# Optimization experiments

Measured on AMD Instinct MI355X. Metric: run time of the kernel, lower is better.

Reference implementation:

```python
import jax, jax.numpy as jnp
import numpy as np

B, S, H, F, E, K, NS = 2, 2048, 2048, 768, 32, 4, 8
SZ = F // NS  # secondary expert size (96)
CAP = 2 * (B * S) * K // E


def setup_inputs() -> dict:
    key = jax.random.key(0)
    k = jax.random.split(key, 7)
    s = 0.02
    return {
        "router_input": jax.random.normal(k[0], (B, S, H), jnp.float32),
        "hidden_states": jax.random.normal(k[1], (B, S, H), jnp.float32),
        "w_router": jax.random.normal(k[2], (H, E), jnp.float32) * s,
        "w_up": jax.random.normal(k[3], (E, H, F), jnp.float32) * s,
        "w_gate": jax.random.normal(k[4], (E, H, F), jnp.float32) * s,
        "w_down": jax.random.normal(k[5], (E, F, H), jnp.float32) * s,
        "w_sgate": jax.random.normal(k[6], (E, H, NS), jnp.float32) * s,
    }


def reference(router_input, hidden_states, w_router, w_up, w_gate, w_down, w_sgate):
    b, s, h = hidden_states.shape
    x = hidden_states.reshape(-1, h)          # [T,H]
    r = router_input.reshape(-1, h)           # [T,H] (early router input)
    T = x.shape[0]

    # top-k routing (early router, softmax over top-k logits)
    logits = r @ w_router                     # [T,E]
    top_logits, sel = jax.lax.top_k(logits, K)  # [T,K]
    rw = jax.nn.softmax(top_logits.astype(jnp.float32), axis=-1).astype(x.dtype)

    # combined per-(expert, token) routing weight and hit mask
    onehot = jax.nn.one_hot(sel, E, dtype=x.dtype)      # [T,K,E]
    wmat = (onehot * rw[..., None]).sum(1).T            # [E,T]
    mask = onehot.sum(1).T                              # [E,T] in {0,1}

    # fixed-capacity dispatch: per expert gather up to CAP routed tokens
    valid, idx = jax.lax.top_k(mask, CAP)               # [E,CAP]
    w = jnp.take_along_axis(wmat, idx, axis=1) * valid  # [E,CAP]

    xe = x[idx]                                         # [E,CAP,H]
    re = r[idx]                                         # [E,CAP,H]

    # hierarchical MLP: secondary gate (hard sigmoid>0.5) over NS groups
    sg = (jax.nn.sigmoid(jnp.einsum('ech,ehs->ecs', re, w_sgate)) > 0.5).astype(x.dtype)
    act = jnp.einsum('ech,ehf->ecf', xe, w_up) * jax.nn.relu(jnp.einsum('ech,ehf->ecf', xe, w_gate))
    act = (act.reshape(E, CAP, NS, SZ) * sg[..., None]).reshape(E, CAP, F)
    out = jnp.einsum('ecf,efh->ech', act, w_down) * w[..., None]  # weighted combine

    # scatter-accumulate back to tokens (invalid slots have zero weight)
    final = jnp.zeros((T, h), x.dtype).at[idx.reshape(-1)].add(out.reshape(-1, h))
    return final.reshape(b, s, h), top_logits
```

## Files before the change

kernel.cpp:

```cpp
#include <hip/hip_runtime.h>

#define TT 4096
#define HD 2048
#define FD 768
#define NE 32
#define TOPK 4
#define NSG 8
#define CAPE 1024
#define MAXTILES 160
#define UPGRID (MAXTILES * 12)
#define DNGRID (MAXTILES * 16)

typedef __attribute__((ext_vector_type(8))) short short8;
typedef __attribute__((ext_vector_type(4))) float f32x4;
typedef __attribute__((ext_vector_type(4))) unsigned short us4;
typedef __attribute__((ext_vector_type(8))) unsigned short us8;

__device__ __forceinline__ unsigned short f2bf(float f) {
  unsigned u = __builtin_bit_cast(unsigned, f);
  u += 0x7FFFu + ((u >> 16) & 1u);
  return (unsigned short)(u >> 16);
}
__device__ __forceinline__ float bf2f(unsigned short b) {
  return __builtin_bit_cast(float, (unsigned)b << 16);
}

__device__ __forceinline__ void async16(const void* g, void* l) {
  __builtin_amdgcn_global_load_lds(
      (const __attribute__((address_space(1))) unsigned int*)g,
      (__attribute__((address_space(3))) unsigned int*)l, 16, 0, 0);
}

__global__ __launch_bounds__(256) void wrt_kernel(const float* __restrict__ w_router,
                                                  float* __restrict__ wrt) {
  int idx = blockIdx.x * 256 + threadIdx.x;
  int e = idx >> 11, h = idx & 2047;
  wrt[idx] = w_router[h * NE + e];
}

#define LSTR 68
__global__ __launch_bounds__(256) void logits_kernel(
    const float* __restrict__ rin, const float* __restrict__ wrt,
    float* __restrict__ logits) {
  __shared__ float As[16 * LSTR];
  __shared__ float Bs[32 * LSTR];
  const int tid = threadIdx.x;
  const int t0 = blockIdx.x * 16;
  const int tp = tid >> 4, eg = tid & 15;
  f32x4 acc0 = (f32x4)0.f, acc1 = (f32x4)0.f;
  for (int kt = 0; kt < HD; kt += 64) {
    __syncthreads();
    {
      int row = tid >> 4, col = (tid & 15) * 4;
      *(f32x4*)&As[row * LSTR + col] =
          *(const f32x4*)&rin[(size_t)(t0 + row) * HD + kt + col];
    }
    {
      int e = tid >> 3, col = (tid & 7) * 8;
      *(f32x4*)&Bs[e * LSTR + col] = *(const f32x4*)&wrt[(size_t)e * HD + kt + col];
      *(f32x4*)&Bs[e * LSTR + col + 4] =
          *(const f32x4*)&wrt[(size_t)e * HD + kt + col + 4];
    }
    __syncthreads();
#pragma unroll
    for (int k4 = 0; k4 < 16; ++k4) {
      f32x4 a = *(const f32x4*)&As[tp * LSTR + k4 * 4];
      f32x4 b0 = *(const f32x4*)&Bs[eg * LSTR + k4 * 4];
      f32x4 b1 = *(const f32x4*)&Bs[(eg + 16) * LSTR + k4 * 4];
      acc0 += a * b0;
      acc1 += a * b1;
    }
  }
  logits[(t0 + tp) * NE + eg] = acc0[0] + acc0[1] + acc0[2] + acc0[3];
  logits[(t0 + tp) * NE + eg + 16] = acc1[0] + acc1[1] + acc1[2] + acc1[3];
}

__global__ __launch_bounds__(256) void topk_kernel(
    const float* __restrict__ logits, float* __restrict__ top_logits,
    int* __restrict__ sel, float* __restrict__ rwts) {
  __shared__ float lg[256 * 33];
  const int tid = threadIdx.x;
  const int t0 = blockIdx.x * 256;
#pragma unroll
  for (int i = 0; i < 8; ++i) {
    int fi = tid + i * 256;
    f32x4 v = *(const f32x4*)&logits[(size_t)t0 * NE + fi * 4];
    int tok = fi >> 3, e0 = (fi & 7) * 4;
#pragma unroll
    for (int c = 0; c < 4; ++c) lg[tok * 33 + e0 + c] = v[c];
  }
  __syncthreads();
  const float* row = &lg[tid * 33];
  float val[TOPK];
  int idx[TOPK];
  unsigned used = 0;
#pragma unroll
  for (int k = 0; k < TOPK; ++k) {
    float best = -1e30f;
    int bi = 0;
    for (int e = 0; e < NE; ++e) {
      float v = row[e];
      if (!((used >> e) & 1u) && v > best) { best = v; bi = e; }
    }
    used |= 1u << bi;
    val[k] = best;
    idx[k] = bi;
  }
  float ex[TOPK], sum = 0.f;
#pragma unroll
  for (int k = 0; k < TOPK; ++k) { ex[k] = expf(val[k] - val[0]); sum += ex[k]; }
  int t = t0 + tid;
#pragma unroll
  for (int k = 0; k < TOPK; ++k) {
    top_logits[t * TOPK + k] = val[k];
    sel[t * TOPK + k] = idx[k];
    rwts[t * TOPK + k] = ex[k] / sum;
  }
}

__global__ __launch_bounds__(256) void dispatch_kernel(
    const int* __restrict__ sel, const float* __restrict__ rwts,
    int* __restrict__ tok_idx, float* __restrict__ tok_w, int* __restrict__ counts,
    int* __restrict__ slotmap) {
  const int e = blockIdx.x;
  __shared__ int wcnt[4];
  __shared__ int base;
  const int tid = threadIdx.x, lane = tid & 63, wid = tid >> 6;
  if (tid == 0) base = 0;
  __syncthreads();
  for (int t0 = 0; t0 < TT; t0 += 256) {
    int t = t0 + tid;
    int hitk = -1;
#pragma unroll
    for (int k = 0; k < TOPK; ++k)
      if (sel[t * TOPK + k] == e) hitk = k;
    unsigned long long m = __ballot(hitk >= 0);
    if (lane == 0) wcnt[wid] = __popcll(m);
    __syncthreads();
    int off = base;
    for (int w = 0; w < wid; ++w) off += wcnt[w];
    int pos = off + __popcll(m & ((1ULL << lane) - 1ULL));
    if (hitk >= 0) {
      if (pos < CAPE) {
        tok_idx[e * CAPE + pos] = t;
        tok_w[e * CAPE + pos] = rwts[t * TOPK + hitk];
        slotmap[t * TOPK + hitk] = e * CAPE + pos;
      } else {
        slotmap[t * TOPK + hitk] = -1;
      }
    }
    __syncthreads();
    if (tid == 0) base += wcnt[0] + wcnt[1] + wcnt[2] + wcnt[3];
    __syncthreads();
  }
  if (tid == 0) counts[e] = base < CAPE ? base : CAPE;
}

__global__ void build_tiles_kernel(const int* __restrict__ counts,
                                   int* __restrict__ tlist, int* __restrict__ ntiles) {
  if (threadIdx.x == 0) {
    int n = 0;
    for (int e = 0; e < NE; ++e) {
      int c = counts[e];
      int mb = (c + 127) >> 7;
      for (int m = 0; m < mb; ++m) tlist[n++] = (e << 8) | m;
    }
    ntiles[0] = n;
  }
}

__global__ __launch_bounds__(256) void sgate_kernel(
    const float* __restrict__ rin, const float* __restrict__ w_sgate,
    const int* __restrict__ tok_idx, const int* __restrict__ counts,
    unsigned* __restrict__ sgbits) {
  const int e = blockIdx.y;
  const int count = counts[e];
  const int s0 = blockIdx.x * 128;
  if (s0 >= count || count == 0) return;
  __shared__ float wsgS[2048 * 9];
  const int tid = threadIdx.x, lane = tid & 63, wid = tid >> 6;
  const float* wsg = w_sgate + (size_t)e * (HD * NSG);
#pragma unroll
  for (int p = 0; p < 8; ++p) {
    int row = p * 256 + tid;
    f32x4 v0 = *(const f32x4*)&wsg[row * 8];
    f32x4 v1 = *(const f32x4*)&wsg[row * 8 + 4];
#pragma unroll
    for (int c = 0; c < 4; ++c) {
      wsgS[row * 9 + c] = v0[c];
      wsgS[row * 9 + 4 + c] = v1[c];
    }
  }
  __syncthreads();
  const int base = s0 + wid * 32;
  for (int j = 0; j < 16; ++j) {
    int sA = base + j, sB = base + j + 16;
    if (sA >= count) break;
    int tokA = tok_idx[e * CAPE + sA];
    int tokB = tok_idx[e * CAPE + (sB < count ? sB : sA)];
    float zA[8], zB[8];
#pragma unroll
    for (int s = 0; s < 8; ++s) { zA[s] = 0.f; zB[s] = 0.f; }
    const float* rAp = rin + (size_t)tokA * HD;
    const float* rBp = rin + (size_t)tokB * HD;
#pragma unroll 4
    for (int i = 0; i < 32; ++i) {
      int h = lane + 64 * i;
      float rA = rAp[h];
      float rB = rBp[h];
#pragma unroll
      for (int s = 0; s < 8; ++s) {
        float w = wsgS[h * 9 + s];
        zA[s] += rA * w;
        zB[s] += rB * w;
      }
    }
#pragma unroll
    for (int s = 0; s < 8; ++s) {
#pragma unroll
      for (int d = 1; d < 64; d <<= 1) {
        zA[s] += __shfl_xor(zA[s], d);
        zB[s] += __shfl_xor(zB[s], d);
      }
    }
    if (lane == 0) {
      unsigned bA = 0, bB = 0;
#pragma unroll
      for (int s = 0; s < 8; ++s) {
        bA |= ((unsigned)(zA[s] > 0.f)) << s;
        bB |= ((unsigned)(zB[s] > 0.f)) << s;
      }
      sgbits[e * CAPE + sA] = bA;
      if (sB < count) sgbits[e * CAPE + sB] = bB;
    }
  }
}

__global__ __launch_bounds__(256) void cvt_x_kernel(const float* __restrict__ x,
                                                    unsigned short* __restrict__ xb) {
  size_t i = ((size_t)blockIdx.x * 256 + threadIdx.x) * 8;
  float4 a = *(const float4*)(x + i);
  float4 b = *(const float4*)(x + i + 4);
  us8 o = {f2bf(a.x), f2bf(a.y), f2bf(a.z), f2bf(a.w),
           f2bf(b.x), f2bf(b.y), f2bf(b.z), f2bf(b.w)};
  *(us8*)(xb + i) = o;
}

__global__ __launch_bounds__(256) void transpose_cvt_kernel(
    const float* __restrict__ in, unsigned short* __restrict__ out, int R, int C) {
  const int e = blockIdx.z;
  const int r0 = blockIdx.x * 64, c0 = blockIdx.y * 64;
  __shared__ float t[64][65];
  const int tid = threadIdx.x;
  const float* inp = in + (size_t)e * R * C;
  {
    const int row = tid >> 4, col4 = (tid & 15) << 2;
#pragma unroll
    for (int p = 0; p < 4; ++p) {
      float4 v = *(const float4*)(inp + (size_t)(r0 + p * 16 + row) * C + c0 + col4);
      t[p * 16 + row][col4 + 0] = v.x;
      t[p * 16 + row][col4 + 1] = v.y;
      t[p * 16 + row][col4 + 2] = v.z;
      t[p * 16 + row][col4 + 3] = v.w;
    }
  }
  __syncthreads();
  {
    const int c = tid >> 2, j = tid & 3;
    us8 o0, o1;
#pragma unroll
    for (int i = 0; i < 8; ++i) o0[i] = f2bf(t[j * 16 + i][c]);
#pragma unroll
    for (int i = 0; i < 8; ++i) o1[i] = f2bf(t[j * 16 + 8 + i][c]);
    unsigned short* op = out + (size_t)e * R * C + (size_t)(c0 + c) * R + r0 + j * 16;
    *(us8*)op = o0;
    *(us8*)(op + 8) = o1;
  }
}

__global__ __launch_bounds__(256, 3) void up_gate_bf16(
    const unsigned short* __restrict__ xb, const unsigned short* __restrict__ wub,
    const unsigned short* __restrict__ wgb, const int* __restrict__ tok_idx,
    const int* __restrict__ counts, const unsigned* __restrict__ sgbits,
    const int* __restrict__ tlist, const int* __restrict__ ntiles,
    unsigned short* __restrict__ act) {
  const int hw = blockIdx.x;
  const int idx = (hw & 7) * (UPGRID / 8) + (hw >> 3);
  const int ti = idx / 12, nb = idx - ti * 12;
  if (ti >= ntiles[0]) return;
  const int entry = tlist[ti];
  const int e = entry >> 8;
  const int m0 = (entry & 255) << 7;
  const int n0 = nb * 64;
  const int count = counts[e];

  __shared__ __align__(16) unsigned short As[128 * 64];
  __shared__ __align__(16) unsigned short Bu[64 * 64];
  __shared__ __align__(16) unsigned short Bg[64 * 64];

  const int tid = threadIdx.x, lane = tid & 63, wid = tid >> 6;
  const int wr = wid >> 1, wc = wid & 1;
  const int ecap = e * CAPE;

  const int srow = tid >> 3, sblk = tid & 7;
  const unsigned short *gA[4], *gU[2], *gG[2];
#pragma unroll
  for (int c = 0; c < 4; ++c) {
    int r = c * 32 + srow;
    int gm = m0 + r;
    int gc = gm < count ? gm : count - 1;
    int swz = (sblk ^ (r & 7)) << 3;
    gA[c] = xb + (size_t)tok_idx[ecap + gc] * HD + swz;
  }
#pragma unroll
  for (int c = 0; c < 2; ++c) {
    int r = c * 32 + srow;
    int swz = (sblk ^ (r & 7)) << 3;
    gU[c] = wub + (size_t)(e * FD + n0 + r) * HD + swz;
    gG[c] = wgb + (size_t)(e * FD + n0 + r) * HD + swz;
  }
  unsigned short* lA = As + (tid << 3);
  unsigned short* lU = Bu + (tid << 3);
  unsigned short* lG = Bg + (tid << 3);

  f32x4 accU[4][2], accG[4][2];
#pragma unroll
  for (int i = 0; i < 4; ++i)
#pragma unroll
    for (int j = 0; j < 2; ++j) { accU[i][j] = (f32x4)0.f; accG[i][j] = (f32x4)0.f; }

  const int fr = lane & 15, fq = lane >> 4;
  const int frx = (fr & 7) << 3;

  for (int kt = 0; kt < HD; kt += 64) {
    __syncthreads();
#pragma unroll
    for (int c = 0; c < 4; ++c) async16(gA[c] + kt, lA + c * 2048);
#pragma unroll
    for (int c = 0; c < 2; ++c) {
      async16(gU[c] + kt, lU + c * 2048);
      async16(gG[c] + kt, lG + c * 2048);
    }
    __syncthreads();
#pragma unroll
    for (int kk = 0; kk < 64; kk += 32) {
      short8 af[4], bu[2], bg[2];
      const int kphys = (kk + fq * 8) ^ frx;
#pragma unroll
      for (int mi = 0; mi < 4; ++mi)
        af[mi] = *(const short8*)(As + ((wr * 64 + mi * 16 + fr) << 6) + kphys);
#pragma unroll
      for (int ni = 0; ni < 2; ++ni) {
        bu[ni] = *(const short8*)(Bu + ((wc * 32 + ni * 16 + fr) << 6) + kphys);
        bg[ni] = *(const short8*)(Bg + ((wc * 32 + ni * 16 + fr) << 6) + kphys);
      }
#pragma unroll
      for (int mi = 0; mi < 4; ++mi)
#pragma unroll
        for (int ni = 0; ni < 2; ++ni) {
          accU[mi][ni] = __builtin_amdgcn_mfma_f32_16x16x32_bf16(af[mi], bu[ni], accU[mi][ni], 0, 0, 0);
          accG[mi][ni] = __builtin_amdgcn_mfma_f32_16x16x32_bf16(af[mi], bg[ni], accG[mi][ni], 0, 0, 0);
        }
    }
  }
#pragma unroll
  for (int mi = 0; mi < 4; ++mi) {
#pragma unroll
    for (int q = 0; q < 4; ++q) {
      int grow = m0 + wr * 64 + mi * 16 + fq * 4 + q;
      if (grow < count) {
        unsigned sg = sgbits[ecap + grow];
        unsigned short* arow = act + (size_t)(ecap + grow) * FD + n0 + wc * 32 + fr;
#pragma unroll
        for (int ni = 0; ni < 2; ++ni) {
          int gcol = n0 + wc * 32 + ni * 16 + fr;
          float a = accU[mi][ni][q] * fmaxf(accG[mi][ni][q], 0.f);
          a = ((sg >> (gcol / 96)) & 1u) ? a : 0.f;
          arow[ni * 16] = f2bf(a);
        }
      }
    }
  }
}

__global__ __launch_bounds__(256, 3) void down_bf16(
    const unsigned short* __restrict__ act, const unsigned short* __restrict__ wdb,
    const int* __restrict__ counts, const int* __restrict__ tlist,
    const int* __restrict__ ntiles, unsigned short* __restrict__ act_dn) {
  const int hw = blockIdx.x;
  const int idx = (hw & 7) * (DNGRID / 8) + (hw >> 3);
  const int ti = idx >> 4, nb = idx & 15;
  if (ti >= ntiles[0]) return;
  const int entry = tlist[ti];
  const int e = entry >> 8;
  const int m0 = (entry & 255) << 7;
  const int n0 = nb * 128;
  const int count = counts[e];

  __shared__ __align__(16) unsigned short As[128 * 64];
  __shared__ __align__(16) unsigned short Bs[128 * 64];

  const int tid = threadIdx.x, lane = tid & 63, wid = tid >> 6;
  const int wr = wid >> 1, wc = wid & 1;
  const int ecap = e * CAPE;

  const int srow = tid >> 3, sblk = tid & 7;
  const unsigned short *gA[4], *gB[4];
#pragma unroll
  for (int c = 0; c < 4; ++c) {
    int r = c * 32 + srow;
    int gr = m0 + r;
    if (gr > CAPE - 1) gr = CAPE - 1;
    int swz = (sblk ^ (r & 7)) << 3;
    gA[c] = act + (size_t)(ecap + gr) * FD + swz;
    gB[c] = wdb + (size_t)(e * HD + n0 + r) * FD + swz;
  }
  unsigned short* lA = As + (tid << 3);
  unsigned short* lB = Bs + (tid << 3);

  f32x4 accD[4][4];
#pragma unroll
  for (int i = 0; i < 4; ++i)
#pragma unroll
    for (int j = 0; j < 4; ++j) accD[i][j] = (f32x4)0.f;

  const int fr = lane & 15, fq = lane >> 4;
  const int frx = (fr & 7) << 3;

  for (int kt = 0; kt < FD; kt += 64) {
    __syncthreads();
#pragma unroll
    for (int c = 0; c < 4; ++c) {
      async16(gA[c] + kt, lA + c * 2048);
      async16(gB[c] + kt, lB + c * 2048);
    }
    __syncthreads();
#pragma unroll
    for (int kk = 0; kk < 64; kk += 32) {
      short8 af[4], bb[4];
      const int kphys = (kk + fq * 8) ^ frx;
#pragma unroll
      for (int mi = 0; mi < 4; ++mi)
        af[mi] = *(const short8*)(As + ((wr * 64 + mi * 16 + fr) << 6) + kphys);
#pragma unroll
      for (int ni = 0; ni < 4; ++ni)
        bb[ni] = *(const short8*)(Bs + ((wc * 64 + ni * 16 + fr) << 6) + kphys);
#pragma unroll
      for (int mi = 0; mi < 4; ++mi)
#pragma unroll
        for (int ni = 0; ni < 4; ++ni)
          accD[mi][ni] = __builtin_amdgcn_mfma_f32_16x16x32_bf16(af[mi], bb[ni], accD[mi][ni], 0, 0, 0);
    }
  }
#pragma unroll
  for (int mi = 0; mi < 4; ++mi) {
#pragma unroll
    for (int q = 0; q < 4; ++q) {
      int grow = m0 + wr * 64 + mi * 16 + fq * 4 + q;
      if (grow < count) {
        unsigned short* drow = act_dn + (size_t)(ecap + grow) * HD + n0 + wc * 64 + fr;
#pragma unroll
        for (int ni = 0; ni < 4; ++ni)
          drow[ni * 16] = f2bf(accD[mi][ni][q]);
      }
    }
  }
}

__global__ __launch_bounds__(256) void combine_kernel(
    const unsigned short* __restrict__ act_dn, const float* __restrict__ tok_w,
    const int* __restrict__ slotmap, float* __restrict__ outF) {
  const int t = blockIdx.x;
  const int h = threadIdx.x * 8;
  const int4 sm = *(const int4*)(slotmap + t * TOPK);
  float acc[8];
#pragma unroll
  for (int j = 0; j < 8; ++j) acc[j] = 0.f;
  const int ss[4] = {sm.x, sm.y, sm.z, sm.w};
#pragma unroll
  for (int k = 0; k < TOPK; ++k) {
    int s = ss[k];
    if (s >= 0) {
      float w = tok_w[s];
      us8 v = *(const us8*)(act_dn + (size_t)s * HD + h);
#pragma unroll
      for (int j = 0; j < 8; ++j) acc[j] += w * bf2f(v[j]);
    }
  }
  float* op = outF + (size_t)t * HD + h;
  f32x4 o0 = {acc[0], acc[1], acc[2], acc[3]};
  f32x4 o1 = {acc[4], acc[5], acc[6], acc[7]};
  *(f32x4*)op = o0;
  *(f32x4*)(op + 4) = o1;
}

extern "C" void kernel_launch(void* const* d_in, const int* in_sizes, int n_in,
                              void* d_out, int out_size, void* d_ws, size_t ws_size,
                              hipStream_t stream) {
  const float* rin = (const float*)d_in[0];
  const float* x = (const float*)d_in[1];
  const float* w_router = (const float*)d_in[2];
  const float* w_up = (const float*)d_in[3];
  const float* w_gate = (const float*)d_in[4];
  const float* w_down = (const float*)d_in[5];
  const float* w_sg = (const float*)d_in[6];
  float* outF = (float*)d_out;
  float* top_logits = outF + (size_t)TT * HD;

  char* ws = (char*)d_ws;
  int* sel = (int*)(ws + 0);
  float* rwts = (float*)(ws + (64 << 10));
  int* tidx = (int*)(ws + (192 << 10));
  float* tw = (float*)(ws + (320 << 10));
  unsigned* sgb = (unsigned*)(ws + (448 << 10));
  int* counts = (int*)(ws + (576 << 10));
  int* tlist = (int*)(ws + (580 << 10));
  int* ntiles = (int*)(ws + (584 << 10));
  float* logits = (float*)(ws + (640 << 10));
  int* slotmap = (int*)(ws + (1152 << 10));
  unsigned short* act = (unsigned short*)(ws + ((size_t)2 << 20));
  float* wrt = (float*)(ws + ((size_t)51 << 20));
  unsigned short* xb = (unsigned short*)(ws + ((size_t)52 << 20));
  unsigned short* wub = (unsigned short*)(ws + ((size_t)69 << 20));
  unsigned short* wgb = wub + (size_t)NE * HD * FD;
  unsigned short* wdb = wgb + (size_t)NE * HD * FD;
  unsigned short* act_dn = wub;

  wrt_kernel<<<256, 256, 0, stream>>>(w_router, wrt);
  logits_kernel<<<TT / 16, 256, 0, stream>>>(rin, wrt, logits);
  topk_kernel<<<TT / 256, 256, 0, stream>>>(logits, top_logits, sel, rwts);
  dispatch_kernel<<<NE, 256, 0, stream>>>(sel, rwts, tidx, tw, counts, slotmap);
  build_tiles_kernel<<<1, 64, 0, stream>>>(counts, tlist, ntiles);
  sgate_kernel<<<dim3(CAPE / 128, NE), 256, 0, stream>>>(rin, w_sg, tidx, counts, sgb);

  cvt_x_kernel<<<(TT * HD) / (256 * 8), 256, 0, stream>>>(x, xb);
  transpose_cvt_kernel<<<dim3(HD / 64, FD / 64, NE), 256, 0, stream>>>(w_up, wub, HD, FD);
  transpose_cvt_kernel<<<dim3(HD / 64, FD / 64, NE), 256, 0, stream>>>(w_gate, wgb, HD, FD);
  transpose_cvt_kernel<<<dim3(FD / 64, HD / 64, NE), 256, 0, stream>>>(w_down, wdb, FD, HD);

  up_gate_bf16<<<UPGRID, 256, 0, stream>>>(xb, wub, wgb, tidx, counts, sgb, tlist, ntiles, act);
  down_bf16<<<DNGRID, 256, 0, stream>>>(act, wdb, counts, tlist, ntiles, act_dn);
  combine_kernel<<<TT, 256, 0, stream>>>(act_dn, tw, slotmap, outF);
}
```

Measured before the change: 574.0 us.

## Double-buffer LDS in expert GEMMs and fuse top-k into router logits kernel

Both expert GEMM kernels (up/gate and down) now use two LDS buffers. The next K-tile is loaded asynchronously while the current one is computed, with explicit vmcnt waits, barriers and raised wave priority around the MFMA section. Separately, router top-k and softmax now run inside the logits kernel from shared memory, which removes one launch and the logits round trip through global memory. Doubling the LDS footprint lowers occupancy (launch bounds go from 3 to 2 blocks), and top-k now runs on only 16 threads per block.

```diff
diff --git a/kernel.cpp b/kernel.cpp
--- a/kernel.cpp
+++ b/kernel.cpp
@@ -41,9 +41,10 @@
 #define LSTR 68
 __global__ __launch_bounds__(256) void logits_kernel(
     const float* __restrict__ rin, const float* __restrict__ wrt,
-    float* __restrict__ logits) {
+    float* __restrict__ top_logits, int* __restrict__ sel, float* __restrict__ rwts) {
   __shared__ float As[16 * LSTR];
   __shared__ float Bs[32 * LSTR];
+  __shared__ float lgS[16][33];
   const int tid = threadIdx.x;
   const int t0 = blockIdx.x * 16;
   const int tp = tid >> 4, eg = tid & 15;
@@ -71,50 +72,36 @@
       acc1 += a * b1;
     }
   }
-  logits[(t0 + tp) * NE + eg] = acc0[0] + acc0[1] + acc0[2] + acc0[3];
-  logits[(t0 + tp) * NE + eg + 16] = acc1[0] + acc1[1] + acc1[2] + acc1[3];
-}
-
-__global__ __launch_bounds__(256) void topk_kernel(
-    const float* __restrict__ logits, float* __restrict__ top_logits,
-    int* __restrict__ sel, float* __restrict__ rwts) {
-  __shared__ float lg[256 * 33];
-  const int tid = threadIdx.x;
-  const int t0 = blockIdx.x * 256;
-#pragma unroll
-  for (int i = 0; i < 8; ++i) {
-    int fi = tid + i * 256;
-    f32x4 v = *(const f32x4*)&logits[(size_t)t0 * NE + fi * 4];
-    int tok = fi >> 3, e0 = (fi & 7) * 4;
-#pragma unroll
-    for (int c = 0; c < 4; ++c) lg[tok * 33 + e0 + c] = v[c];
-  }
+  lgS[tp][eg] = acc0[0] + acc0[1] + acc0[2] + acc0[3];
+  lgS[tp][eg + 16] = acc1[0] + acc1[1] + acc1[2] + acc1[3];
   __syncthreads();
-  const float* row = &lg[tid * 33];
-  float val[TOPK];
-  int idx[TOPK];
-  unsigned used = 0;
-#pragma unroll
-  for (int k = 0; k < TOPK; ++k) {
-    float best = -1e30f;
-    int bi = 0;
-    for (int e = 0; e < NE; ++e) {
-      float v = row[e];
-      if (!((used >> e) & 1u) && v > best) { best = v; bi = e; }
-    }
-    used |= 1u << bi;
-    val[k] = best;
-    idx[k] = bi;
-  }
-  float ex[TOPK], sum = 0.f;
-#pragma unroll
-  for (int k = 0; k < TOPK; ++k) { ex[k] = expf(val[k] - val[0]); sum += ex[k]; }
-  int t = t0 + tid;
-#pragma unroll
-  for (int k = 0; k < TOPK; ++k) {
-    top_logits[t * TOPK + k] = val[k];
-    sel[t * TOPK + k] = idx[k];
-    rwts[t * TOPK + k] = ex[k] / sum;
+  if (tid < 16) {
+    const float* row = lgS[tid];
+    float val[TOPK];
+    int idx[TOPK];
+    unsigned used = 0;
+#pragma unroll
+    for (int k = 0; k < TOPK; ++k) {
+      float best = -1e30f;
+      int bi = 0;
+      for (int e = 0; e < NE; ++e) {
+        float v = row[e];
+        if (!((used >> e) & 1u) && v > best) { best = v; bi = e; }
+      }
+      used |= 1u << bi;
+      val[k] = best;
+      idx[k] = bi;
+    }
+    float ex[TOPK], sum = 0.f;
+#pragma unroll
+    for (int k = 0; k < TOPK; ++k) { ex[k] = expf(val[k] - val[0]); sum += ex[k]; }
+    int t = t0 + tid;
+#pragma unroll
+    for (int k = 0; k < TOPK; ++k) {
+      top_logits[t * TOPK + k] = val[k];
+      sel[t * TOPK + k] = idx[k];
+      rwts[t * TOPK + k] = ex[k] / sum;
+    }
   }
 }
 
@@ -278,7 +265,7 @@
   }
 }
 
-__global__ __launch_bounds__(256, 3) void up_gate_bf16(
+__global__ __launch_bounds__(256, 2) void up_gate_bf16(
     const unsigned short* __restrict__ xb, const unsigned short* __restrict__ wub,
     const unsigned short* __restrict__ wgb, const int* __restrict__ tok_idx,
     const int* __restrict__ counts, const unsigned* __restrict__ sgbits,
@@ -294,9 +281,9 @@
   const int n0 = nb * 64;
   const int count = counts[e];
 
-  __shared__ __align__(16) unsigned short As[128 * 64];
-  __shared__ __align__(16) unsigned short Bu[64 * 64];
-  __shared__ __align__(16) unsigned short Bg[64 * 64];
+  __shared__ __align__(16) unsigned short As0[128 * 64], As1[128 * 64];
+  __shared__ __align__(16) unsigned short Bu0[64 * 64], Bu1[64 * 64];
+  __shared__ __align__(16) unsigned short Bg0[64 * 64], Bg1[64 * 64];
 
   const int tid = threadIdx.x, lane = tid & 63, wid = tid >> 6;
   const int wr = wid >> 1, wc = wid & 1;
@@ -319,9 +306,6 @@
     gU[c] = wub + (size_t)(e * FD + n0 + r) * HD + swz;
     gG[c] = wgb + (size_t)(e * FD + n0 + r) * HD + swz;
   }
-  unsigned short* lA = As + (tid << 3);
-  unsigned short* lU = Bu + (tid << 3);
-  unsigned short* lG = Bg + (tid << 3);
 
   f32x4 accU[4][2], accG[4][2];
 #pragma unroll
@@ -331,28 +315,30 @@
 
   const int fr = lane & 15, fq = lane >> 4;
   const int frx = (fr & 7) << 3;
-
-  for (int kt = 0; kt < HD; kt += 64) {
-    __syncthreads();
-#pragma unroll
-    for (int c = 0; c < 4; ++c) async16(gA[c] + kt, lA + c * 2048);
+  const int toff = tid << 3;
+
+  auto stage = [&](unsigned short* A_, unsigned short* U_, unsigned short* G_, int kt) {
+#pragma unroll
+    for (int c = 0; c < 4; ++c) async16(gA[c] + kt, A_ + toff + c * 2048);
 #pragma unroll
     for (int c = 0; c < 2; ++c) {
-      async16(gU[c] + kt, lU + c * 2048);
-      async16(gG[c] + kt, lG + c * 2048);
-    }
-    __syncthreads();
+      async16(gU[c] + kt, U_ + toff + c * 2048);
+      async16(gG[c] + kt, G_ + toff + c * 2048);
+    }
+  };
+  auto compute = [&](const unsigned short* A_, const unsigned short* U_,
+                     const unsigned short* G_) {
 #pragma unroll
     for (int kk = 0; kk < 64; kk += 32) {
       short8 af[4], bu[2], bg[2];
       const int kphys = (kk + fq * 8) ^ frx;
 #pragma unroll
       for (int mi = 0; mi < 4; ++mi)
-        af[mi] = *(const short8*)(As + ((wr * 64 + mi * 16 + fr) << 6) + kphys);
+        af[mi] = *(const short8*)(A_ + ((wr * 64 + mi * 16 + fr) << 6) + kphys);
 #pragma unroll
       for (int ni = 0; ni < 2; ++ni) {
-        bu[ni] = *(const short8*)(Bu + ((wc * 32 + ni * 16 + fr) << 6) + kphys);
-        bg[ni] = *(const short8*)(Bg + ((wc * 32 + ni * 16 + fr) << 6) + kphys);
+        bu[ni] = *(const short8*)(U_ + ((wc * 32 + ni * 16 + fr) << 6) + kphys);
+        bg[ni] = *(const short8*)(G_ + ((wc * 32 + ni * 16 + fr) << 6) + kphys);
       }
 #pragma unroll
       for (int mi = 0; mi < 4; ++mi)
@@ -362,7 +348,34 @@
           accG[mi][ni] = __builtin_amdgcn_mfma_f32_16x16x32_bf16(af[mi], bg[ni], accG[mi][ni], 0, 0, 0);
         }
     }
-  }
+  };
+
+  stage(As0, Bu0, Bg0, 0);
+  for (int kt = 0; kt < HD; kt += 128) {
+    stage(As1, Bu1, Bg1, kt + 64);
+    asm volatile("s_waitcnt vmcnt(8)" ::: "memory");
+    __builtin_amdgcn_s_barrier();
+    __builtin_amdgcn_sched_barrier(0);
+    __builtin_amdgcn_s_setprio(1);
+    compute(As0, Bu0, Bg0);
+    __builtin_amdgcn_s_setprio(0);
+    __builtin_amdgcn_sched_barrier(0);
+    __builtin_amdgcn_s_barrier();
+    if (kt + 128 < HD) {
+      stage(As0, Bu0, Bg0, kt + 128);
+      asm volatile("s_waitcnt vmcnt(8)" ::: "memory");
+    } else {
+      asm volatile("s_waitcnt vmcnt(0)" ::: "memory");
+    }
+    __builtin_amdgcn_s_barrier();
+    __builtin_amdgcn_sched_barrier(0);
+    __builtin_amdgcn_s_setprio(1);
+    compute(As1, Bu1, Bg1);
+    __builtin_amdgcn_s_setprio(0);
+    __builtin_amdgcn_sched_barrier(0);
+    __builtin_amdgcn_s_barrier();
+  }
+
 #pragma unroll
   for (int mi = 0; mi < 4; ++mi) {
 #pragma unroll
@@ -383,7 +396,7 @@
   }
 }
 
-__global__ __launch_bounds__(256, 3) void down_bf16(
+__global__ __launch_bounds__(256, 2) void down_bf16(
     const unsigned short* __restrict__ act, const unsigned short* __restrict__ wdb,
     const int* __restrict__ counts, const int* __restrict__ tlist,
     const int* __restrict__ ntiles, unsigned short* __restrict__ act_dn) {
@@ -397,8 +410,8 @@
   const int n0 = nb * 128;
   const int count = counts[e];
 
-  __shared__ __align__(16) unsigned short As[128 * 64];
-  __shared__ __align__(16) unsigned short Bs[128 * 64];
+  __shared__ __align__(16) unsigned short As0[128 * 64], As1[128 * 64];
+  __shared__ __align__(16) unsigned short Bs0[128 * 64], Bs1[128 * 64];
 
   const int tid = threadIdx.x, lane = tid & 63, wid = tid >> 6;
   const int wr = wid >> 1, wc = wid & 1;
@@ -415,8 +428,6 @@
     gA[c] = act + (size_t)(ecap + gr) * FD + swz;
     gB[c] = wdb + (size_t)(e * HD + n0 + r) * FD + swz;
   }
-  unsigned short* lA = As + (tid << 3);
-  unsigned short* lB = Bs + (tid << 3);
 
   f32x4 accD[4][4];
 #pragma unroll
@@ -426,32 +437,60 @@
 
   const int fr = lane & 15, fq = lane >> 4;
   const int frx = (fr & 7) << 3;
-
-  for (int kt = 0; kt < FD; kt += 64) {
-    __syncthreads();
+  const int toff = tid << 3;
+
+  auto stage = [&](unsigned short* A_, unsigned short* B_, int kt) {
 #pragma unroll
     for (int c = 0; c < 4; ++c) {
-      async16(gA[c] + kt, lA + c * 2048);
-      async16(gB[c] + kt, lB + c * 2048);
-    }
-    __syncthreads();
+      async16(gA[c] + kt, A_ + toff + c * 2048);
+      async16(gB[c] + kt, B_ + toff + c * 2048);
+    }
+  };
+  auto compute = [&](const unsigned short* A_, const unsigned short* B_) {
 #pragma unroll
     for (int kk = 0; kk < 64; kk += 32) {
       short8 af[4], bb[4];
       const int kphys = (kk + fq * 8) ^ frx;
 #pragma unroll
       for (int mi = 0; mi < 4; ++mi)
-        af[mi] = *(const short8*)(As + ((wr * 64 + mi * 16 + fr) << 6) + kphys);
+        af[mi] = *(const short8*)(A_ + ((wr * 64 + mi * 16 + fr) << 6) + kphys);
 #pragma unroll
       for (int ni = 0; ni < 4; ++ni)
-        bb[ni] = *(const short8*)(Bs + ((wc * 64 + ni * 16 + fr) << 6) + kphys);
+        bb[ni] = *(const short8*)(B_ + ((wc * 64 + ni * 16 + fr) << 6) + kphys);
 #pragma unroll
       for (int mi = 0; mi < 4; ++mi)
 #pragma unroll
         for (int ni = 0; ni < 4; ++ni)
           accD[mi][ni] = __builtin_amdgcn_mfma_f32_16x16x32_bf16(af[mi], bb[ni], accD[mi][ni], 0, 0, 0);
     }
-  }
+  };
+
+  stage(As0, Bs0, 0);
+  for (int kt = 0; kt < FD; kt += 128) {
+    stage(As1, Bs1, kt + 64);
+    asm volatile("s_waitcnt vmcnt(8)" ::: "memory");
+    __builtin_amdgcn_s_barrier();
+    __builtin_amdgcn_sched_barrier(0);
+    __builtin_amdgcn_s_setprio(1);
+    compute(As0, Bs0);
+    __builtin_amdgcn_s_setprio(0);
+    __builtin_amdgcn_sched_barrier(0);
+    __builtin_amdgcn_s_barrier();
+    if (kt + 128 < FD) {
+      stage(As0, Bs0, kt + 128);
+      asm volatile("s_waitcnt vmcnt(8)" ::: "memory");
+    } else {
+      asm volatile("s_waitcnt vmcnt(0)" ::: "memory");
+    }
+    __builtin_amdgcn_s_barrier();
+    __builtin_amdgcn_sched_barrier(0);
+    __builtin_amdgcn_s_setprio(1);
+    compute(As1, Bs1);
+    __builtin_amdgcn_s_setprio(0);
+    __builtin_amdgcn_sched_barrier(0);
+    __builtin_amdgcn_s_barrier();
+  }
+
 #pragma unroll
   for (int mi = 0; mi < 4; ++mi) {
 #pragma unroll
@@ -516,7 +555,6 @@
   int* counts = (int*)(ws + (576 << 10));
   int* tlist = (int*)(ws + (580 << 10));
   int* ntiles = (int*)(ws + (584 << 10));
-  float* logits = (float*)(ws + (640 << 10));
   int* slotmap = (int*)(ws + (1152 << 10));
   unsigned short* act = (unsigned short*)(ws + ((size_t)2 << 20));
   float* wrt = (float*)(ws + ((size_t)51 << 20));
@@ -527,8 +565,7 @@
   unsigned short* act_dn = wub;
 
   wrt_kernel<<<256, 256, 0, stream>>>(w_router, wrt);
-  logits_kernel<<<TT / 16, 256, 0, stream>>>(rin, wrt, logits);
-  topk_kernel<<<TT / 256, 256, 0, stream>>>(logits, top_logits, sel, rwts);
+  logits_kernel<<<TT / 16, 256, 0, stream>>>(rin, wrt, top_logits, sel, rwts);
   dispatch_kernel<<<NE, 256, 0, stream>>>(sel, rwts, tidx, tw, counts, slotmap);
   build_tiles_kernel<<<1, 64, 0, stream>>>(counts, tlist, ntiles);
   sgate_kernel<<<dim3(CAPE / 128, NE), 256, 0, stream>>>(rin, w_sg, tidx, counts, sgb);
```

Measured after the change: 616.4 us. 1.07x slower.
